# Optimization experiments

Hardware: AMD Instinct MI355X
Metric: run time of the kernel (lower is better)

## Reference

```python
import jax, jax.numpy as jnp
import numpy as np

N = 50000      # nodes
E = 800000     # edges (avg degree 16)
LM = 1024      # lm_dim
H = 128        # hidden_channels
OUT = 64       # out_channels


def setup_inputs() -> dict:
    key = jax.random.key(0)
    ks = jax.random.split(key, 13)
    s = 0.02
    return {
        "x": jax.random.normal(ks[0], (N,), dtype=jnp.float32),
        "x_out": jax.random.normal(ks[1], (N, LM), dtype=jnp.float32),
        "c": jax.random.normal(ks[2], (N,), dtype=jnp.float32),
        "edge_index": jax.random.randint(ks[3], (2, E), 0, N, dtype=jnp.int64),
        "edge_weight": jax.random.uniform(ks[4], (E,), dtype=jnp.float32),
        # weights stored as [in, out]
        "Wa": jax.random.normal(ks[5], (1, LM), dtype=jnp.float32) * s,   # aa_linear (no bias)
        "Wc": jax.random.normal(ks[6], (1, LM), dtype=jnp.float32) * s,   # c_linear (no bias)
        "Wl": jax.random.normal(ks[7], (LM, LM), dtype=jnp.float32) * s,  # lm_linear
        "bl": jax.random.normal(ks[8], (LM,), dtype=jnp.float32) * s,
        "W1": jax.random.normal(ks[9], (LM, H), dtype=jnp.float32) * s,   # conv1
        "b1": jax.random.normal(ks[10], (H,), dtype=jnp.float32) * s,
        "W3": jax.random.normal(ks[11], (H, OUT), dtype=jnp.float32) * s,  # conv3
        "b3": jax.random.normal(ks[12], (OUT,), dtype=jnp.float32) * s,
    }


def gcn_conv(h, src, dst, ew, W, b, n):
    """PyG GCNConv with normalize=True, add_self_loops=True."""
    h = h @ W                                   # [n, out]
    loop = jnp.arange(n, dtype=src.dtype)
    src_f = jnp.concatenate([src, loop])
    dst_f = jnp.concatenate([dst, loop])
    ew_f = jnp.concatenate([ew, jnp.ones((n,), ew.dtype)])
    deg = jax.ops.segment_sum(ew_f, dst_f, num_segments=n)     # in-degree incl. self-loops
    dis = jnp.where(deg > 0, jax.lax.rsqrt(deg), 0.0)          # deg^{-1/2}
    norm = dis[src_f] * ew_f * dis[dst_f]                      # per-edge coefficient
    out = jax.ops.segment_sum(norm[:, None] * h[src_f], dst_f, num_segments=n)
    return out + b


def reference(x, x_out, c, edge_index, edge_weight, Wa, Wc, Wl, bl, W1, b1, W3, b3):
    # (c_linear(c[:,None]) + aa_linear(x[:,None]) + lm_linear(x_out)).relu()
    h = jax.nn.relu(c[:, None] * Wc[0] + x[:, None] * Wa[0] + x_out @ Wl + bl)  # [N, LM]
    src, dst = edge_index[0], edge_index[1]
    h = jax.nn.relu(gcn_conv(h, src, dst, edge_weight, W1, b1, N))              # [N, H]
    return gcn_conv(h, src, dst, edge_weight, W3, b3, N)                        # [N, OUT]
```

## Files before the change

### kernel.cpp

```cpp
#include <hip/hip_runtime.h>
#include <hip/hip_bf16.h>

typedef unsigned short u16;
typedef unsigned long long u64;
typedef __attribute__((ext_vector_type(8))) short bf16x8;
typedef __attribute__((ext_vector_type(4))) float f32x4;

constexpr int NN = 50000;
constexpr int NE = 800000;
constexpr int LM = 1024;
constexpr int HC = 128;
constexpr int OC = 64;

constexpr size_t OFF_ROWPTR = 0;
constexpr size_t OFF_CURSOR = 200192;
constexpr size_t OFF_PK     = 400384;
constexpr size_t OFF_INCL   = 800512;
constexpr size_t OFF_BSUM   = 1000704;
constexpr size_t OFF_DIS    = 1000960;
constexpr size_t OFF_META   = 1201152;
constexpr size_t OFF_WLT    = 7601408;
constexpr size_t OFF_W1T    = 9698560;
constexpr size_t OFF_H      = 9960704;
constexpr size_t OFF_Y1     = 112360704;
constexpr size_t OFF_Y3     = 125160704;
constexpr size_t OFF_ABF    = 131560704;
constexpr size_t NEED_FAST  = OFF_ABF + (size_t)NN * LM * 2;

constexpr size_t CVT_TOTAL = (size_t)NN * LM / 8;
constexpr size_t CVT_CNT   = 2560000;
constexpr size_t CVT_SC1   = 1280000;
constexpr size_t CVT_SC3   = 640000;
constexpr size_t CVT_FIL   = 1920000;

__device__ __forceinline__ u16 f2bf(float f) {
    union { float f; unsigned int u; } a; a.f = f;
    unsigned int u = a.u + 0x7FFFu + ((a.u >> 16) & 1u);
    return (u16)(u >> 16);
}
__device__ __forceinline__ float bf2f(u16 v) {
    union { unsigned int u; float f; } a; a.u = ((unsigned int)v) << 16;
    return a.f;
}
__device__ __forceinline__ ushort2 pkbf(float a, float b) {
    union { __hip_bfloat162 h; ushort2 u; } cv;
    cv.h = __float22bfloat162_rn(make_float2(a, b));
    return cv.u;
}
__device__ __forceinline__ void async_copy16(u16* lds, const u16* g) {
    __builtin_amdgcn_global_load_lds(
        (const __attribute__((address_space(1))) void*)g,
        (__attribute__((address_space(3))) void*)lds, 16, 0, 0);
}
__device__ __forceinline__ void cvt_chunk(size_t idx, const float* __restrict__ A32,
                                          u16* __restrict__ Abf) {
    const float* src = A32 + idx * 8;
    float4 v0 = *(const float4*)(src);
    float4 v1 = *(const float4*)(src + 4);
    union { ushort2 u2[4]; bf16x8 v; } pk2;
    pk2.u2[0] = pkbf(v0.x, v0.y);
    pk2.u2[1] = pkbf(v0.z, v0.w);
    pk2.u2[2] = pkbf(v1.x, v1.y);
    pk2.u2[3] = pkbf(v1.z, v1.w);
    *(bf16x8*)(Abf + idx * 8) = pk2.v;
}

__global__ void k_count(const int* __restrict__ ei, const float* __restrict__ ew,
                        u64* __restrict__ pk,
                        const float* __restrict__ Wl, u16* __restrict__ WlT,
                        const float* __restrict__ W1, u16* __restrict__ W1T,
                        const float* __restrict__ A32, u16* __restrict__ Abf) {
    int b = blockIdx.x, t = threadIdx.x;
    if (b < 3125) {
        int e = b * 256 + t;
        if (e < NE) {
            int d = ei[NE + e];
            u64 add = (1ULL << 48) | (u64)(ew[e] * 4294967296.0);
            atomicAdd(&pk[d], add);
        }
    } else if (b < 4149) {
        __shared__ float sm[32][33];
        int bb = b - 3125;
        int n0 = (bb & 31) * 32, k0 = (bb >> 5) * 32;
        int ty = t >> 5, tx = t & 31;
        #pragma unroll
        for (int i = 0; i < 4; i++)
            sm[ty + i * 8][tx] = Wl[(size_t)(k0 + ty + i * 8) * LM + n0 + tx];
        __syncthreads();
        #pragma unroll
        for (int i = 0; i < 4; i++)
            WlT[(size_t)(n0 + ty + i * 8) * LM + k0 + tx] = f2bf(sm[tx][ty + i * 8]);
    } else if (b < 4661) {
        int idx = (b - 4149) * 256 + t;
        if (idx < HC * LM) {
            int o = idx >> 10, k = idx & 1023;
            W1T[idx] = f2bf(W1[(size_t)k * HC + o]);
        }
    } else {
        cvt_chunk((size_t)(b - 4661) * 256 + t, A32, Abf);
    }
}

__global__ void k_scan1(const u64* __restrict__ pk, int* __restrict__ incl,
                        int* __restrict__ bsum,
                        const float* __restrict__ A32, u16* __restrict__ Abf) {
    int b = blockIdx.x, t = threadIdx.x;
    if (b >= 49) {
        cvt_chunk(CVT_CNT + (size_t)(b - 49) * 1024 + t, A32, Abf);
        return;
    }
    __shared__ int sm[1024];
    int idx = b * 1024 + t;
    int v = (idx < NN) ? (int)(pk[idx] >> 48) : 0;
    sm[t] = v; __syncthreads();
    for (int off = 1; off < 1024; off <<= 1) {
        int add = (t >= off) ? sm[t - off] : 0;
        __syncthreads();
        sm[t] += add;
        __syncthreads();
    }
    if (idx < NN) incl[idx] = sm[t];
    if (t == 1023) bsum[b] = sm[t];
}

__global__ void k_scan3(const int* __restrict__ incl, const u64* __restrict__ pk,
                        const int* __restrict__ bsum,
                        int* __restrict__ rowptr, int* __restrict__ cursor,
                        float* __restrict__ dis,
                        const float* __restrict__ A32, u16* __restrict__ Abf) {
    int b = blockIdx.x;
    if (b >= 196) {
        cvt_chunk(CVT_CNT + CVT_SC1 + (size_t)(b - 196) * 256 + threadIdx.x, A32, Abf);
        return;
    }
    int seg = b >> 2;
    int lane = threadIdx.x & 63;
    int v = (lane < seg) ? bsum[lane] : 0;
    #pragma unroll
    for (int off = 32; off > 0; off >>= 1) v += __shfl_down(v, off, 64);
    int boffv = __shfl(v, 0, 64);
    int idx = b * 256 + threadIdx.x;
    if (idx < NN) {
        u64 p = pk[idx];
        int cnt = (int)(p >> 48);
        float deg = (float)((double)(p & 0xFFFFFFFFFFFFULL) * 2.3283064365386963e-10);
        int rp = incl[idx] - cnt + boffv;
        rowptr[idx] = rp;
        cursor[idx] = rp;
        dis[idx] = rsqrtf(1.0f + deg);
    } else if (idx == NN) {
        rowptr[NN] = NE;
    }
}

__global__ void k_fill(const int* __restrict__ ei, const float* __restrict__ ew,
                       const float* __restrict__ dis,
                       int* __restrict__ cursor, int2* __restrict__ meta,
                       const float* __restrict__ A32, u16* __restrict__ Abf) {
    int b = blockIdx.x;
    if (b >= 3125) {
        cvt_chunk(CVT_CNT + CVT_SC1 + CVT_SC3 + (size_t)(b - 3125) * 256 + threadIdx.x,
                  A32, Abf);
        return;
    }
    int e = b * 256 + threadIdx.x;
    if (e < NE) {
        int s = ei[e];
        int d = ei[NE + e];
        int slot = atomicAdd(&cursor[d], 1);
        meta[slot] = make_int2(s, __float_as_int(ew[e] * dis[s]));
    }
}

__global__ __launch_bounds__(256, 2) void k_gemm1a(
    const u16* __restrict__ Abf, const u16* __restrict__ Bt, u16* __restrict__ Cout,
    const float* __restrict__ xv, const float* __restrict__ cv,
    const float* __restrict__ Wa, const float* __restrict__ Wc,
    const float* __restrict__ bl) {
    __shared__ u16 lA[128 * 64];
    __shared__ u16 lB[128 * 64];
    const int tid = threadIdx.x;
    const int lane = tid & 63, wv = tid >> 6;
    int x = blockIdx.x & 7, j = blockIdx.x >> 3;
    int bx = (j & ~7) | x;
    int by = j & 7;
    if (bx >= 391) return;
    const int m0 = bx * 128, n0 = by * 128;
    const int wm = (wv >> 1) * 64, wn = (wv & 1) * 64;
    const int fr = lane & 15, qd = lane >> 4;

    f32x4 acc[4][4] = {};

    for (int kt = 0; kt < 16; kt++) {
        const int k0 = kt << 6;
        __syncthreads();
        #pragma unroll
        for (int i = 0; i < 4; i++) {
            int r0 = i * 32 + wv * 8;
            int rl = r0 + (lane >> 3);
            int slot = lane & 7;
            int k8 = slot ^ (rl & 7);
            const u16* g = Bt + (size_t)(n0 + rl) * LM + k0 + k8 * 8;
            async_copy16(&lB[r0 * 64], g);
        }
        #pragma unroll
        for (int i = 0; i < 4; i++) {
            int r0 = i * 32 + wv * 8;
            int rl = r0 + (lane >> 3);
            int slot = lane & 7;
            int k8 = slot ^ (rl & 7);
            int row = m0 + rl; if (row >= NN) row = NN - 1;
            const u16* g = Abf + (size_t)row * LM + k0 + k8 * 8;
            async_copy16(&lA[r0 * 64], g);
        }
        __syncthreads();
        #pragma unroll
        for (int s = 0; s < 2; s++) {
            const int slot = (s * 4 + qd) ^ (fr & 7);
            bf16x8 af[4], bfm[4];
            #pragma unroll
            for (int mi = 0; mi < 4; mi++)
                af[mi] = *(const bf16x8*)&lA[(wm + mi * 16 + fr) * 64 + slot * 8];
            #pragma unroll
            for (int ni = 0; ni < 4; ni++)
                bfm[ni] = *(const bf16x8*)&lB[(wn + ni * 16 + fr) * 64 + slot * 8];
            #pragma unroll
            for (int mi = 0; mi < 4; mi++)
                #pragma unroll
                for (int ni = 0; ni < 4; ni++)
                    acc[mi][ni] = __builtin_amdgcn_mfma_f32_16x16x32_bf16(
                        af[mi], bfm[ni], acc[mi][ni], 0, 0, 0);
        }
    }

    int jj[4]; float waj[4], wcj[4], blj[4];
    #pragma unroll
    for (int ni = 0; ni < 4; ni++) {
        jj[ni] = n0 + wn + ni * 16 + fr;
        waj[ni] = Wa[jj[ni]]; wcj[ni] = Wc[jj[ni]]; blj[ni] = bl[jj[ni]];
    }
    #pragma unroll
    for (int mi = 0; mi < 4; mi++)
        #pragma unroll
        for (int r = 0; r < 4; r++) {
            int row = m0 + wm + mi * 16 + qd * 4 + r;
            if (row < NN) {
                float xb = xv[row], cb = cv[row];
                #pragma unroll
                for (int ni = 0; ni < 4; ni++) {
                    float v = acc[mi][ni][r] + xb * waj[ni] + cb * wcj[ni] + blj[ni];
                    Cout[(size_t)row * LM + jj[ni]] = f2bf(fmaxf(v, 0.f));
                }
            }
        }
}

__global__ __launch_bounds__(256, 2) void k_gemm1f(
    const float* __restrict__ A32, const u16* __restrict__ Bt, u16* __restrict__ Cout,
    const float* __restrict__ xv, const float* __restrict__ cv,
    const float* __restrict__ Wa, const float* __restrict__ Wc,
    const float* __restrict__ bl) {
    __shared__ u16 lA[128 * 64];
    __shared__ u16 lB[2][128 * 64];
    const int tid = threadIdx.x;
    const int lane = tid & 63, wv = tid >> 6;
    const int bx = ((blockIdx.x >> 5) << 3) | (blockIdx.x & 7);
    const int by = (blockIdx.x >> 3) & 3;
    if (bx >= 391) return;
    const int m0 = bx * 128, n0 = by * 256;
    const int wm = (wv >> 1) * 64, wn = (wv & 1) * 64;
    const int fr = lane & 15, qd = lane >> 4;

    f32x4 acc[2][4][4] = {};

    int srl[4], sslot[4]; const float* sbase[4];
    float4 pf[8];
    #pragma unroll
    for (int i = 0; i < 4; i++) {
        int cidx = i * 256 + tid;
        srl[i] = cidx >> 3; sslot[i] = cidx & 7;
        int k8 = sslot[i] ^ (srl[i] & 7);
        int row = m0 + srl[i]; if (row >= NN) row = NN - 1;
        sbase[i] = A32 + (size_t)row * LM + k8 * 8;
    }
    #pragma unroll
    for (int i = 0; i < 4; i++) {
        pf[2 * i]     = *(const float4*)(sbase[i]);
        pf[2 * i + 1] = *(const float4*)(sbase[i] + 4);
    }

    for (int kt = 0; kt < 16; kt++) {
        const int k0 = kt << 6;
        __syncthreads();
        #pragma unroll
        for (int h = 0; h < 2; h++)
            #pragma unroll
            for (int i = 0; i < 4; i++) {
                int r0 = i * 32 + wv * 8;
                int rl = r0 + (lane >> 3);
                int slot = lane & 7;
                int k8 = slot ^ (rl & 7);
                const u16* g = Bt + (size_t)(n0 + h * 128 + rl) * LM + k0 + k8 * 8;
                async_copy16(&lB[h][r0 * 64], g);
            }
        #pragma unroll
        for (int i = 0; i < 4; i++) {
            union { ushort2 u2[4]; bf16x8 v; } pk;
            pk.u2[0] = pkbf(pf[2 * i].x, pf[2 * i].y);
            pk.u2[1] = pkbf(pf[2 * i].z, pf[2 * i].w);
            pk.u2[2] = pkbf(pf[2 * i + 1].x, pf[2 * i + 1].y);
            pk.u2[3] = pkbf(pf[2 * i + 1].z, pf[2 * i + 1].w);
            *(bf16x8*)&lA[srl[i] * 64 + sslot[i] * 8] = pk.v;
        }
        __syncthreads();
        if (kt < 15) {
            #pragma unroll
            for (int i = 0; i < 4; i++) {
                pf[2 * i]     = *(const float4*)(sbase[i] + k0 + 64);
                pf[2 * i + 1] = *(const float4*)(sbase[i] + k0 + 68);
            }
        }
        #pragma unroll
        for (int s = 0; s < 2; s++) {
            const int slot = (s * 4 + qd) ^ (fr & 7);
            bf16x8 af[4];
            #pragma unroll
            for (int mi = 0; mi < 4; mi++)
                af[mi] = *(const bf16x8*)&lA[(wm + mi * 16 + fr) * 64 + slot * 8];
            #pragma unroll
            for (int h = 0; h < 2; h++) {
                bf16x8 bfm[4];
                #pragma unroll
                for (int ni = 0; ni < 4; ni++)
                    bfm[ni] = *(const bf16x8*)&lB[h][(wn + ni * 16 + fr) * 64 + slot * 8];
                #pragma unroll
                for (int mi = 0; mi < 4; mi++)
                    #pragma unroll
                    for (int ni = 0; ni < 4; ni++)
                        acc[h][mi][ni] = __builtin_amdgcn_mfma_f32_16x16x32_bf16(
                            af[mi], bfm[ni], acc[h][mi][ni], 0, 0, 0);
            }
        }
    }

    #pragma unroll
    for (int h = 0; h < 2; h++) {
        int jj[4]; float waj[4], wcj[4], blj[4];
        #pragma unroll
        for (int ni = 0; ni < 4; ni++) {
            jj[ni] = n0 + h * 128 + wn + ni * 16 + fr;
            waj[ni] = Wa[jj[ni]]; wcj[ni] = Wc[jj[ni]]; blj[ni] = bl[jj[ni]];
        }
        #pragma unroll
        for (int mi = 0; mi < 4; mi++)
            #pragma unroll
            for (int r = 0; r < 4; r++) {
                int row = m0 + wm + mi * 16 + qd * 4 + r;
                if (row < NN) {
                    float xb = xv[row], cb = cv[row];
                    #pragma unroll
                    for (int ni = 0; ni < 4; ni++) {
                        float v = acc[h][mi][ni][r] + xb * waj[ni] + cb * wcj[ni] + blj[ni];
                        Cout[(size_t)row * LM + jj[ni]] = f2bf(fmaxf(v, 0.f));
                    }
                }
            }
    }
}

__global__ __launch_bounds__(256) void k_gemm2(
    const u16* __restrict__ Abf, const u16* __restrict__ Bt, u16* __restrict__ Cout) {
    __shared__ u16 lA[64 * 64];
    __shared__ u16 lB[128 * 64];
    const int tid = threadIdx.x;
    const int lane = tid & 63, wv = tid >> 6;
    const int m0 = blockIdx.x * 64;
    const int wm = (wv >> 1) * 32, wn = (wv & 1) * 64;
    const int fr = lane & 15, qd = lane >> 4;
    f32x4 acc[2][4] = {};

    for (int kt = 0; kt < 16; kt++) {
        const int k0 = kt << 6;
        __syncthreads();
        #pragma unroll
        for (int i = 0; i < 4; i++) {
            int r0 = i * 32 + wv * 8;
            int rl = r0 + (lane >> 3);
            int slot = lane & 7;
            int k8 = slot ^ (rl & 7);
            const u16* g = Bt + (size_t)rl * LM + k0 + k8 * 8;
            async_copy16(&lB[r0 * 64], g);
        }
        #pragma unroll
        for (int i = 0; i < 2; i++) {
            int r0 = i * 32 + wv * 8;
            int rl = r0 + (lane >> 3);
            int slot = lane & 7;
            int k8 = slot ^ (rl & 7);
            int row = m0 + rl; if (row >= NN) row = NN - 1;
            const u16* g = Abf + (size_t)row * LM + k0 + k8 * 8;
            async_copy16(&lA[r0 * 64], g);
        }
        __syncthreads();
        #pragma unroll
        for (int s = 0; s < 2; s++) {
            const int slot = (s * 4 + qd) ^ (fr & 7);
            bf16x8 af[2], bfm[4];
            #pragma unroll
            for (int mi = 0; mi < 2; mi++)
                af[mi] = *(const bf16x8*)&lA[(wm + mi * 16 + fr) * 64 + slot * 8];
            #pragma unroll
            for (int ni = 0; ni < 4; ni++)
                bfm[ni] = *(const bf16x8*)&lB[(wn + ni * 16 + fr) * 64 + slot * 8];
            #pragma unroll
            for (int mi = 0; mi < 2; mi++)
                #pragma unroll
                for (int ni = 0; ni < 4; ni++)
                    acc[mi][ni] = __builtin_amdgcn_mfma_f32_16x16x32_bf16(
                        af[mi], bfm[ni], acc[mi][ni], 0, 0, 0);
        }
    }
    #pragma unroll
    for (int mi = 0; mi < 2; mi++)
        #pragma unroll
        for (int r = 0; r < 4; r++) {
            int row = m0 + wm + mi * 16 + qd * 4 + r;
            if (row < NN) {
                #pragma unroll
                for (int ni = 0; ni < 4; ni++)
                    Cout[(size_t)row * HC + wn + ni * 16 + fr] = f2bf(acc[mi][ni][r]);
            }
        }
}

__global__ __launch_bounds__(512) void k_agg1g3(
    const u16* __restrict__ y1, const int* __restrict__ rowptr,
    const int2* __restrict__ meta, const float* __restrict__ dis,
    const float* __restrict__ b1, const float* __restrict__ W3,
    u16* __restrict__ y3) {
    __shared__ float hrow[8][HC];
    __shared__ float w3s[HC * OC];
    const int tid = threadIdx.x;
    const int wv = tid >> 6, lane = tid & 63;
    #pragma unroll
    for (int i = 0; i < 16; i++) w3s[i * 512 + tid] = W3[i * 512 + tid];
    int node = blockIdx.x * 8 + wv;
    float di = dis[node];
    int p0 = rowptr[node], p1 = rowptr[node + 1];
    ushort2 sv = *(const ushort2*)(y1 + (size_t)node * HC + lane * 2);
    float a0 = di * bf2f(sv.x), a1 = di * bf2f(sv.y);
    #pragma unroll 8
    for (int p = p0; p < p1; ++p) {
        int2 m = meta[p];
        float nm = __int_as_float(m.y);
        ushort2 v = *(const ushort2*)(y1 + (size_t)m.x * HC + lane * 2);
        a0 += nm * bf2f(v.x);
        a1 += nm * bf2f(v.y);
    }
    a0 = fmaxf(di * a0 + b1[lane * 2], 0.f);
    a1 = fmaxf(di * a1 + b1[lane * 2 + 1], 0.f);
    hrow[wv][lane * 2] = a0;
    hrow[wv][lane * 2 + 1] = a1;
    __syncthreads();
    if (wv < 2) {
        const int nb = wv * 4;
        float c0 = 0.f, c1 = 0.f, c2 = 0.f, c3 = 0.f;
        #pragma unroll 4
        for (int k = 0; k < HC; ++k) {
            float w = w3s[k * OC + lane];
            c0 += hrow[nb][k] * w;
            c1 += hrow[nb + 1][k] * w;
            c2 += hrow[nb + 2][k] * w;
            c3 += hrow[nb + 3][k] * w;
        }
        size_t base = (size_t)(blockIdx.x * 8 + nb) * OC + lane;
        y3[base]          = f2bf(c0);
        y3[base + OC]     = f2bf(c1);
        y3[base + 2 * OC] = f2bf(c2);
        y3[base + 3 * OC] = f2bf(c3);
    }
}

__global__ __launch_bounds__(256) void k_agg3(
    const u16* __restrict__ y3, const int* __restrict__ rowptr,
    const int2* __restrict__ meta, const float* __restrict__ dis,
    const float* __restrict__ b3, float* __restrict__ outp) {
    int node = blockIdx.x * 4 + (threadIdx.x >> 6);
    int lane = threadIdx.x & 63;
    if (node >= NN) return;
    float di = dis[node];
    int p0 = rowptr[node], p1 = rowptr[node + 1];
    float a = di * bf2f(y3[(size_t)node * OC + lane]);
    #pragma unroll 8
    for (int p = p0; p < p1; ++p) {
        int2 m = meta[p];
        a += __int_as_float(m.y) * bf2f(y3[(size_t)m.x * OC + lane]);
    }
    outp[(size_t)node * OC + lane] = di * a + b3[lane];
}

extern "C" void kernel_launch(void* const* d_in, const int* in_sizes, int n_in,
                              void* d_out, int out_size, void* d_ws, size_t ws_size,
                              hipStream_t stream) {
    const float* x    = (const float*)d_in[0];
    const float* xout = (const float*)d_in[1];
    const float* c    = (const float*)d_in[2];
    const int*   ei   = (const int*)d_in[3];
    const float* ew   = (const float*)d_in[4];
    const float* Wa   = (const float*)d_in[5];
    const float* Wc   = (const float*)d_in[6];
    const float* Wl   = (const float*)d_in[7];
    const float* bl   = (const float*)d_in[8];
    const float* W1   = (const float*)d_in[9];
    const float* b1   = (const float*)d_in[10];
    const float* W3   = (const float*)d_in[11];
    const float* b3   = (const float*)d_in[12];
    float* outp = (float*)d_out;

    char* ws = (char*)d_ws;
    int*   rowptr = (int*)(ws + OFF_ROWPTR);
    int*   cursor = (int*)(ws + OFF_CURSOR);
    u64*   pk     = (u64*)(ws + OFF_PK);
    int*   incl   = (int*)(ws + OFF_INCL);
    int*   bsum   = (int*)(ws + OFF_BSUM);
    float* dis    = (float*)(ws + OFF_DIS);
    int2*  meta   = (int2*)(ws + OFF_META);
    u16*   WlT    = (u16*)(ws + OFF_WLT);
    u16*   W1T    = (u16*)(ws + OFF_W1T);
    u16*   hbuf   = (u16*)(ws + OFF_H);
    u16*   y1     = (u16*)(ws + OFF_Y1);
    u16*   y3     = (u16*)(ws + OFF_Y3);
    u16*   Abf    = (u16*)(ws + OFF_ABF);

    const bool fast = (ws_size >= NEED_FAST);

    hipMemsetAsync(pk, 0, (size_t)NN * sizeof(u64), stream);
    k_count<<<fast ? 14661 : 4661, 256, 0, stream>>>(ei, ew, pk, Wl, WlT, W1, W1T,
                                                     xout, Abf);
    k_scan1<<<fast ? 1299 : 49, 1024, 0, stream>>>(pk, incl, bsum, xout, Abf);
    k_scan3<<<fast ? 2696 : 196, 256, 0, stream>>>(incl, pk, bsum, rowptr, cursor,
                                                   dis, xout, Abf);
    k_fill <<<fast ? 10625 : 3125, 256, 0, stream>>>(ei, ew, dis, cursor, meta,
                                                     xout, Abf);

    if (fast) {
        k_gemm1a<<<392 * 8, 256, 0, stream>>>(Abf, WlT, hbuf, x, c, Wa, Wc, bl);
    } else {
        k_gemm1f<<<49 * 32, 256, 0, stream>>>(xout, WlT, hbuf, x, c, Wa, Wc, bl);
    }
    k_gemm2<<<782, 256, 0, stream>>>(hbuf, W1T, y1);
    k_agg1g3<<<6250, 512, 0, stream>>>(y1, rowptr, meta, dis, b1, W3, y3);
    k_agg3<<<12500, 256, 0, stream>>>(y3, rowptr, meta, dis, b3, outp);
}
```

Measured before the change: 632.6 us.

## Fold CSR scan stages into GEMM launches and vectorize edge count/fill

Moves the per-block degree scan into extra blocks of the first GEMM launch and the rowptr/dis computation into extra blocks of the second GEMM launch. The full x_out bf16 conversion now happens in the count kernel instead of being spread across the scan and fill kernels. The count and fill kernels process four edges per thread with vector loads. This cuts the number of kernel launches and lets the small graph-preprocessing work run alongside the GEMMs. In exchange, the conversion is concentrated in one large launch, and fill now runs after gemm2 on the critical path.

```diff
diff --git a/kernel.cpp b/kernel.cpp
--- a/kernel.cpp
+++ b/kernel.cpp
@@ -27,12 +27,6 @@
 constexpr size_t OFF_ABF    = 131560704;
 constexpr size_t NEED_FAST  = OFF_ABF + (size_t)NN * LM * 2;
 
-constexpr size_t CVT_TOTAL = (size_t)NN * LM / 8;
-constexpr size_t CVT_CNT   = 2560000;
-constexpr size_t CVT_SC1   = 1280000;
-constexpr size_t CVT_SC3   = 640000;
-constexpr size_t CVT_FIL   = 1920000;
-
 __device__ __forceinline__ u16 f2bf(float f) {
     union { float f; unsigned int u; } a; a.f = f;
     unsigned int u = a.u + 0x7FFFu + ((a.u >> 16) & 1u);
@@ -65,81 +59,50 @@
     *(bf16x8*)(Abf + idx * 8) = pk2.v;
 }
 
-__global__ void k_count(const int* __restrict__ ei, const float* __restrict__ ew,
-                        u64* __restrict__ pk,
-                        const float* __restrict__ Wl, u16* __restrict__ WlT,
-                        const float* __restrict__ W1, u16* __restrict__ W1T,
-                        const float* __restrict__ A32, u16* __restrict__ Abf) {
-    int b = blockIdx.x, t = threadIdx.x;
-    if (b < 3125) {
-        int e = b * 256 + t;
-        if (e < NE) {
-            int d = ei[NE + e];
-            u64 add = (1ULL << 48) | (u64)(ew[e] * 4294967296.0);
-            atomicAdd(&pk[d], add);
-        }
-    } else if (b < 4149) {
-        __shared__ float sm[32][33];
-        int bb = b - 3125;
-        int n0 = (bb & 31) * 32, k0 = (bb >> 5) * 32;
-        int ty = t >> 5, tx = t & 31;
-        #pragma unroll
-        for (int i = 0; i < 4; i++)
-            sm[ty + i * 8][tx] = Wl[(size_t)(k0 + ty + i * 8) * LM + n0 + tx];
-        __syncthreads();
-        #pragma unroll
-        for (int i = 0; i < 4; i++)
-            WlT[(size_t)(n0 + ty + i * 8) * LM + k0 + tx] = f2bf(sm[tx][ty + i * 8]);
-    } else if (b < 4661) {
-        int idx = (b - 4149) * 256 + t;
-        if (idx < HC * LM) {
-            int o = idx >> 10, k = idx & 1023;
-            W1T[idx] = f2bf(W1[(size_t)k * HC + o]);
-        }
-    } else {
-        cvt_chunk((size_t)(b - 4661) * 256 + t, A32, Abf);
-    }
-}
-
-__global__ void k_scan1(const u64* __restrict__ pk, int* __restrict__ incl,
-                        int* __restrict__ bsum,
-                        const float* __restrict__ A32, u16* __restrict__ Abf) {
-    int b = blockIdx.x, t = threadIdx.x;
-    if (b >= 49) {
-        cvt_chunk(CVT_CNT + (size_t)(b - 49) * 1024 + t, A32, Abf);
-        return;
-    }
-    __shared__ int sm[1024];
-    int idx = b * 1024 + t;
-    int v = (idx < NN) ? (int)(pk[idx] >> 48) : 0;
-    sm[t] = v; __syncthreads();
-    for (int off = 1; off < 1024; off <<= 1) {
-        int add = (t >= off) ? sm[t - off] : 0;
-        __syncthreads();
-        sm[t] += add;
-        __syncthreads();
-    }
-    if (idx < NN) incl[idx] = sm[t];
-    if (t == 1023) bsum[b] = sm[t];
-}
-
-__global__ void k_scan3(const int* __restrict__ incl, const u64* __restrict__ pk,
-                        const int* __restrict__ bsum,
-                        int* __restrict__ rowptr, int* __restrict__ cursor,
-                        float* __restrict__ dis,
-                        const float* __restrict__ A32, u16* __restrict__ Abf) {
-    int b = blockIdx.x;
-    if (b >= 196) {
-        cvt_chunk(CVT_CNT + CVT_SC1 + (size_t)(b - 196) * 256 + threadIdx.x, A32, Abf);
-        return;
-    }
+__device__ __forceinline__ void scan1_body(int b, int t, const u64* __restrict__ pk,
+                                           int* __restrict__ incl,
+                                           int* __restrict__ bsum) {
+    __shared__ int ssc[256];
+    int base = b * 1024 + t * 4;
+    int v[4], s = 0;
+    #pragma unroll
+    for (int i = 0; i < 4; i++) {
+        int idx = base + i;
+        v[i] = (idx < NN) ? (int)(pk[idx] >> 48) : 0;
+        s += v[i];
+    }
+    int mytot = s;
+    ssc[t] = mytot; __syncthreads();
+    for (int off = 1; off < 256; off <<= 1) {
+        int add = (t >= off) ? ssc[t - off] : 0;
+        __syncthreads();
+        ssc[t] += add;
+        __syncthreads();
+    }
+    int prev = ssc[t] - mytot;
+    int run = 0;
+    #pragma unroll
+    for (int i = 0; i < 4; i++) {
+        run += v[i];
+        int idx = base + i;
+        if (idx < NN) incl[idx] = prev + run;
+    }
+    if (t == 255) bsum[b] = ssc[255];
+}
+
+__device__ __forceinline__ void scan3_body(int b, int t, const int* __restrict__ incl,
+                                           const u64* __restrict__ pk,
+                                           const int* __restrict__ bsum,
+                                           int* __restrict__ rowptr,
+                                           int* __restrict__ cursor,
+                                           float* __restrict__ dis) {
     int seg = b >> 2;
-    int lane = threadIdx.x & 63;
+    int lane = t & 63;
     int v = (lane < seg) ? bsum[lane] : 0;
     #pragma unroll
     for (int off = 32; off > 0; off >>= 1) v += __shfl_down(v, off, 64);
     int boffv = __shfl(v, 0, 64);
-    int idx = b * 256 + threadIdx.x;
+    int idx = b * 256 + t;
     if (idx < NN) {
         u64 p = pk[idx];
         int cnt = (int)(p >> 48);
@@ -153,22 +116,73 @@
     }
 }
 
+__global__ void k_count(const int* __restrict__ ei, const float* __restrict__ ew,
+                        u64* __restrict__ pk,
+                        const float* __restrict__ Wl, u16* __restrict__ WlT,
+                        const float* __restrict__ W1, u16* __restrict__ W1T,
+                        const float* __restrict__ A32, u16* __restrict__ Abf) {
+    int b = blockIdx.x, t = threadIdx.x;
+    if (b < 782) {
+        int e0 = (b * 256 + t) * 4;
+        if (e0 < NE) {
+            int4 d4 = *(const int4*)(ei + NE + e0);
+            float4 w4 = *(const float4*)(ew + e0);
+            atomicAdd(&pk[d4.x], (1ULL << 48) | (u64)(w4.x * 4294967296.0));
+            atomicAdd(&pk[d4.y], (1ULL << 48) | (u64)(w4.y * 4294967296.0));
+            atomicAdd(&pk[d4.z], (1ULL << 48) | (u64)(w4.z * 4294967296.0));
+            atomicAdd(&pk[d4.w], (1ULL << 48) | (u64)(w4.w * 4294967296.0));
+        }
+    } else if (b < 1806) {
+        __shared__ float sm[32][33];
+        int bb = b - 782;
+        int n0 = (bb & 31) * 32, k0 = (bb >> 5) * 32;
+        int ty = t >> 5, tx = t & 31;
+        #pragma unroll
+        for (int i = 0; i < 4; i++)
+            sm[ty + i * 8][tx] = Wl[(size_t)(k0 + ty + i * 8) * LM + n0 + tx];
+        __syncthreads();
+        #pragma unroll
+        for (int i = 0; i < 4; i++)
+            WlT[(size_t)(n0 + ty + i * 8) * LM + k0 + tx] = f2bf(sm[tx][ty + i * 8]);
+    } else if (b < 2318) {
+        int idx = (b - 1806) * 256 + t;
+        if (idx < HC * LM) {
+            int o = idx >> 10, k = idx & 1023;
+            W1T[idx] = f2bf(W1[(size_t)k * HC + o]);
+        }
+    } else {
+        cvt_chunk((size_t)(b - 2318) * 256 + t, A32, Abf);
+    }
+}
+
+__global__ void k_scan1s(const u64* __restrict__ pk, int* __restrict__ incl,
+                         int* __restrict__ bsum) {
+    scan1_body(blockIdx.x, threadIdx.x, pk, incl, bsum);
+}
+__global__ void k_scan3s(const int* __restrict__ incl, const u64* __restrict__ pk,
+                         const int* __restrict__ bsum,
+                         int* __restrict__ rowptr, int* __restrict__ cursor,
+                         float* __restrict__ dis) {
+    scan3_body(blockIdx.x, threadIdx.x, incl, pk, bsum, rowptr, cursor, dis);
+}
+
 __global__ void k_fill(const int* __restrict__ ei, const float* __restrict__ ew,
                        const float* __restrict__ dis,
-                       int* __restrict__ cursor, int2* __restrict__ meta,
-                       const float* __restrict__ A32, u16* __restrict__ Abf) {
-    int b = blockIdx.x;
-    if (b >= 3125) {
-        cvt_chunk(CVT_CNT + CVT_SC1 + CVT_SC3 + (size_t)(b - 3125) * 256 + threadIdx.x,
-                  A32, Abf);
-        return;
-    }
-    int e = b * 256 + threadIdx.x;
-    if (e < NE) {
-        int s = ei[e];
-        int d = ei[NE + e];
-        int slot = atomicAdd(&cursor[d], 1);
-        meta[slot] = make_int2(s, __float_as_int(ew[e] * dis[s]));
+                       int* __restrict__ cursor, int2* __restrict__ meta) {
+    int e0 = (blockIdx.x * 256 + threadIdx.x) * 4;
+    if (e0 < NE) {
+        int4 s4 = *(const int4*)(ei + e0);
+        int4 d4 = *(const int4*)(ei + NE + e0);
+        float4 w4 = *(const float4*)(ew + e0);
+        int slot;
+        slot = atomicAdd(&cursor[d4.x], 1);
+        meta[slot] = make_int2(s4.x, __float_as_int(w4.x * dis[s4.x]));
+        slot = atomicAdd(&cursor[d4.y], 1);
+        meta[slot] = make_int2(s4.y, __float_as_int(w4.y * dis[s4.y]));
+        slot = atomicAdd(&cursor[d4.z], 1);
+        meta[slot] = make_int2(s4.z, __float_as_int(w4.z * dis[s4.z]));
+        slot = atomicAdd(&cursor[d4.w], 1);
+        meta[slot] = make_int2(s4.w, __float_as_int(w4.w * dis[s4.w]));
     }
 }
 
@@ -176,12 +190,18 @@
     const u16* __restrict__ Abf, const u16* __restrict__ Bt, u16* __restrict__ Cout,
     const float* __restrict__ xv, const float* __restrict__ cv,
     const float* __restrict__ Wa, const float* __restrict__ Wc,
-    const float* __restrict__ bl) {
+    const float* __restrict__ bl,
+    const u64* __restrict__ pk, int* __restrict__ incl, int* __restrict__ bsum) {
+    if (blockIdx.x < 49) {
+        scan1_body(blockIdx.x, threadIdx.x, pk, incl, bsum);
+        return;
+    }
     __shared__ u16 lA[128 * 64];
     __shared__ u16 lB[128 * 64];
     const int tid = threadIdx.x;
     const int lane = tid & 63, wv = tid >> 6;
-    int x = blockIdx.x & 7, j = blockIdx.x >> 3;
+    const int g = blockIdx.x - 49;
+    int x = g & 7, j = g >> 3;
     int bx = (j & ~7) | x;
     int by = j & 7;
     if (bx >= 391) return;
@@ -200,8 +220,8 @@
             int rl = r0 + (lane >> 3);
             int slot = lane & 7;
             int k8 = slot ^ (rl & 7);
-            const u16* g = Bt + (size_t)(n0 + rl) * LM + k0 + k8 * 8;
-            async_copy16(&lB[r0 * 64], g);
+            const u16* gp = Bt + (size_t)(n0 + rl) * LM + k0 + k8 * 8;
+            async_copy16(&lB[r0 * 64], gp);
         }
         #pragma unroll
         for (int i = 0; i < 4; i++) {
@@ -210,8 +230,8 @@
             int slot = lane & 7;
             int k8 = slot ^ (rl & 7);
             int row = m0 + rl; if (row >= NN) row = NN - 1;
-            const u16* g = Abf + (size_t)row * LM + k0 + k8 * 8;
-            async_copy16(&lA[r0 * 64], g);
+            const u16* gp = Abf + (size_t)row * LM + k0 + k8 * 8;
+            async_copy16(&lA[r0 * 64], gp);
         }
         __syncthreads();
         #pragma unroll
@@ -369,12 +389,19 @@
 }
 
 __global__ __launch_bounds__(256) void k_gemm2(
-    const u16* __restrict__ Abf, const u16* __restrict__ Bt, u16* __restrict__ Cout) {
+    const u16* __restrict__ Abf, const u16* __restrict__ Bt, u16* __restrict__ Cout,
+    int nscan, const int* __restrict__ incl, const u64* __restrict__ pk,
+    const int* __restrict__ bsum, int* __restrict__ rowptr,
+    int* __restrict__ cursor, float* __restrict__ dis) {
+    if (blockIdx.x < nscan) {
+        scan3_body(blockIdx.x, threadIdx.x, incl, pk, bsum, rowptr, cursor, dis);
+        return;
+    }
     __shared__ u16 lA[64 * 64];
     __shared__ u16 lB[128 * 64];
     const int tid = threadIdx.x;
     const int lane = tid & 63, wv = tid >> 6;
-    const int m0 = blockIdx.x * 64;
+    const int m0 = (blockIdx.x - nscan) * 64;
     const int wm = (wv >> 1) * 32, wn = (wv & 1) * 64;
     const int fr = lane & 15, qd = lane >> 4;
     f32x4 acc[2][4] = {};
@@ -535,20 +562,23 @@
     const bool fast = (ws_size >= NEED_FAST);
 
     hipMemsetAsync(pk, 0, (size_t)NN * sizeof(u64), stream);
-    k_count<<<fast ? 14661 : 4661, 256, 0, stream>>>(ei, ew, pk, Wl, WlT, W1, W1T,
-                                                     xout, Abf);
-    k_scan1<<<fast ? 1299 : 49, 1024, 0, stream>>>(pk, incl, bsum, xout, Abf);
-    k_scan3<<<fast ? 2696 : 196, 256, 0, stream>>>(incl, pk, bsum, rowptr, cursor,
-                                                   dis, xout, Abf);
-    k_fill <<<fast ? 10625 : 3125, 256, 0, stream>>>(ei, ew, dis, cursor, meta,
-                                                     xout, Abf);
 
     if (fast) {
-        k_gemm1a<<<392 * 8, 256, 0, stream>>>(Abf, WlT, hbuf, x, c, Wa, Wc, bl);
+        k_count<<<27318, 256, 0, stream>>>(ei, ew, pk, Wl, WlT, W1, W1T, xout, Abf);
+        k_gemm1a<<<49 + 392 * 8, 256, 0, stream>>>(Abf, WlT, hbuf, x, c, Wa, Wc, bl,
+                                                   pk, incl, bsum);
+        k_gemm2<<<196 + 782, 256, 0, stream>>>(hbuf, W1T, y1, 196, incl, pk, bsum,
+                                               rowptr, cursor, dis);
+        k_fill<<<782, 256, 0, stream>>>(ei, ew, dis, cursor, meta);
     } else {
+        k_count<<<2318, 256, 0, stream>>>(ei, ew, pk, Wl, WlT, W1, W1T, xout, Abf);
+        k_scan1s<<<49, 256, 0, stream>>>(pk, incl, bsum);
+        k_scan3s<<<196, 256, 0, stream>>>(incl, pk, bsum, rowptr, cursor, dis);
+        k_fill<<<782, 256, 0, stream>>>(ei, ew, dis, cursor, meta);
         k_gemm1f<<<49 * 32, 256, 0, stream>>>(xout, WlT, hbuf, x, c, Wa, Wc, bl);
-    }
-    k_gemm2<<<782, 256, 0, stream>>>(hbuf, W1T, y1);
+        k_gemm2<<<782, 256, 0, stream>>>(hbuf, W1T, y1, 0, incl, pk, bsum,
+                                         rowptr, cursor, dis);
+    }
     k_agg1g3<<<6250, 512, 0, stream>>>(y1, rowptr, meta, dis, b1, W3, y3);
     k_agg3<<<12500, 256, 0, stream>>>(y3, rowptr, meta, dis, b3, outp);
 }
```

After: 639.9 us. Within noise of the previous version (+1.2%).
